# Performance work log

Hardware: AMD Instinct MI355X
Metric: run time of the kernel (lower is better)

## Reference

```python
import jax, jax.numpy as jnp
import numpy as np
from jax import lax

GAMMA = 1.0
BIG = 1e8  # matches the torch init value 100000000.0


def setup_inputs() -> dict:
    key = jax.random.key(0)
    k1, k2 = jax.random.split(key)
    B, n, m, d = 256, 256, 256, 32
    x = jax.random.normal(k1, (B, n, d), dtype=jnp.float32)
    y = jax.random.normal(k2, (B, m, d), dtype=jnp.float32)
    return {"x": x, "y": y}


def _soft_dtw(x, y, gamma):
    B, n, d = x.shape
    m = y.shape[1]
    # squared euclidean distances, (B, n, m); GEMM form avoids the (B,n,m,d) blowup
    x2 = jnp.sum(x * x, axis=-1)
    y2 = jnp.sum(y * y, axis=-1)
    dist = x2[:, :, None] + y2[:, None, :] - 2.0 * jnp.einsum('bnd,bmd->bnm', x, y)
    dist = jnp.maximum(dist, 0.0)  # cdist(p=2)**2 is nonnegative

    def softmin3(a, b, c):
        s = jnp.stack([a, b, c], axis=0)
        return -gamma * jax.nn.logsumexp(-s / gamma, axis=0)

    big_col = jnp.full((B,), BIG, dtype=x.dtype)

    def row_step(prev_row, d_row):
        # prev_row: (B, m+1) = D[i-1, :];  d_row: (B, m) = dist[:, i-1, :]
        def col_step(cur, inp):
            # cur: (B,) = D[i, j-1]; inp: (dist[i-1,j-1], D[i-1,j], D[i-1,j-1])
            dij, up, diag = inp
            new = dij + softmin3(up, cur, diag)
            return new, new
        xs = (d_row.T, prev_row[:, 1:].T, prev_row[:, :-1].T)  # each (m, B)
        _, vals = lax.scan(col_step, big_col, xs)  # vals: (m, B)
        new_row = jnp.concatenate([big_col[:, None], vals.T], axis=1)  # (B, m+1)
        return new_row, None

    init_row = jnp.concatenate(
        [jnp.zeros((B, 1), x.dtype), jnp.full((B, m), BIG, dtype=x.dtype)], axis=1)
    final_row, _ = lax.scan(row_step, init_row, jnp.swapaxes(dist, 0, 1))  # scan over n rows
    return jnp.mean(final_row[:, m])


def reference(x, y):
    return _soft_dtw(x, y, GAMMA)
```

## Files before the change

kernel.cpp:

```cpp
#include <hip/hip_runtime.h>

#define BIG 1e8f
#define LN2 0.69314718f
#define LOG2E 1.44269504f
#define M2L -2.8853900818f

#define RSLOT 112
#define DRB 1040

#define OFF_XH   116480
#define OFF_X2S  132864
#define OFF_Y2S  133888
#define OFF_RDY  134912
#define OFF_PRG  134976
#define LDS_BYTES 135040

typedef _Float16 half8 __attribute__((ext_vector_type(8)));
typedef _Float16 half2_t __attribute__((ext_vector_type(2)));
typedef float f32x4 __attribute__((ext_vector_type(4)));

__device__ __forceinline__ float exp2g(float x) {
#if __has_builtin(__builtin_amdgcn_exp2f)
    return __builtin_amdgcn_exp2f(x);
#else
    return exp2f(x);
#endif
}
__device__ __forceinline__ float log2g(float x) {
#if __has_builtin(__builtin_amdgcn_logf)
    return __builtin_amdgcn_logf(x);
#else
    return log2f(x);
#endif
}

__device__ __forceinline__ half2_t pkrtz(float a, float b) {
    return __builtin_bit_cast(half2_t, __builtin_amdgcn_cvt_pkrtz(a, b));
}

__device__ __forceinline__ void pairp(float a, float b, float& m, float& s) {
    m = fminf(a, b);
    s = exp2g(-fabsf(a - b)) + 1.f;
}
__device__ __forceinline__ float smp(float m, float s, float v) {
    float d = v - m;
    float t = exp2g(-fabsf(d));
    float r = (d > 0.f) ? (t + s) : fmaf(s, t, 1.f);
    return fminf(m, v) - log2g(r);
}

__device__ __forceinline__ float shfl_up1(float v, float oldv) {
    int r = __builtin_amdgcn_update_dpp(
        __builtin_bit_cast(int, oldv), __builtin_bit_cast(int, v),
        0x138 , 0xf, 0xf, false);
    return __builtin_bit_cast(float, r);
}

__device__ __forceinline__ void dec2(unsigned int w, float& a, float& b) {
    half2_t h = __builtin_bit_cast(half2_t, w);
    a = (float)h[0];
    b = (float)h[1];
}

__global__ __launch_bounds__(128, 1) void sdtw_kernel(
    const float* __restrict__ x, const float* __restrict__ y,
    float* __restrict__ out) {
    extern __shared__ __align__(16) char smem[];
    unsigned char* band = (unsigned char*)smem;
    _Float16* xh = (_Float16*)(smem + OFF_XH);
    float* x2sL = (float*)(smem + OFF_X2S);
    float* y2sL = (float*)(smem + OFF_Y2S);
    volatile int* rdy = (volatile int*)(smem + OFF_RDY);
    volatile int* prg = (volatile int*)(smem + OFF_PRG);

    const int tid = threadIdx.x;
    const int b = blockIdx.x;
    const float* xb = x + (size_t)b * 8192;
    const float* yb = y + (size_t)b * 8192;

#pragma unroll
    for (int rr = 0; rr < 2; rr++) {
        const int r = tid + rr * 128;
        const float4* px = (const float4*)(xb + r * 32);
        union { _Float16 h[32]; half8 v[4]; } uc;
        float s2 = 0.f;
#pragma unroll
        for (int q = 0; q < 8; q++) {
            float4 f = px[q];
            s2 += f.x * f.x + f.y * f.y + f.z * f.z + f.w * f.w;
            uc.h[4 * q + 0] = (_Float16)f.x;
            uc.h[4 * q + 1] = (_Float16)f.y;
            uc.h[4 * q + 2] = (_Float16)f.z;
            uc.h[4 * q + 3] = (_Float16)f.w;
        }
        half8* dst = (half8*)&xh[r * 32];
#pragma unroll
        for (int q = 0; q < 4; q++) dst[q] = uc.v[q];
        x2sL[r] = s2 * LOG2E;

        const float4* py = (const float4*)(yb + r * 32);
        float t2 = 0.f;
#pragma unroll
        for (int q = 0; q < 8; q++) {
            float4 f = py[q];
            t2 += f.x * f.x + f.y * f.y + f.z * f.z + f.w * f.w;
        }
        y2sL[r] = t2 * LOG2E;
    }
    if (tid < 16) rdy[tid] = 0;
    if (tid == 16) *prg = 0;
    __syncthreads();

    if (tid >= 64) {
        const int lane = tid - 64;
        const int qd = lane >> 4, xr = lane & 15;

        half8 yfrag[16];
        float yvL[16];
#pragma unroll
        for (int ci = 0; ci < 16; ci++) {
            const float* yp = yb + (ci * 16 + xr) * 32 + qd * 8;
            float4 f0 = *(const float4*)yp;
            float4 f1 = *(const float4*)(yp + 4);
            half8 v;
            v[0] = (_Float16)f0.x; v[1] = (_Float16)f0.y;
            v[2] = (_Float16)f0.z; v[3] = (_Float16)f0.w;
            v[4] = (_Float16)f1.x; v[5] = (_Float16)f1.y;
            v[6] = (_Float16)f1.z; v[7] = (_Float16)f1.w;
            yfrag[ci] = v;
            yvL[ci] = y2sL[ci * 16 + xr];
        }

        for (int sg = 0; sg < 16; sg++) {
            if (sg >= 6) {
                const int need = 8 * sg - 40;
                while (*prg < need) {}
            }
            const half8 xf = *(const half8*)&xh[(sg * 16 + xr) * 32 + qd * 8];
            const float4 xl = *(const float4*)&x2sL[sg * 16 + qd * 4];
            const int p0 = 8 * sg + 2 * qd;
#pragma unroll
            for (int ci = 0; ci < 16; ci++) {
                f32x4 acc = {0.f, 0.f, 0.f, 0.f};
                acc = __builtin_amdgcn_mfma_f32_16x16x32_f16(xf, yfrag[ci], acc, 0, 0, 0);
                const int c = ci * 16 + xr;
                const float yv = yvL[ci];
                const float d0 = fmaxf(fmaf(M2L, acc[0], xl.x + yv), 0.f);
                const float d1 = fmaxf(fmaf(M2L, acc[1], xl.y + yv), 0.f);
                const float d2 = fmaxf(fmaf(M2L, acc[2], xl.z + yv), 0.f);
                const float d3 = fmaxf(fmaf(M2L, acc[3], xl.w + yv), 0.f);
                const half2_t h01 = pkrtz(d0, d1);
                const half2_t h23 = pkrtz(d2, d3);
                const int dr0 = p0 + (c >> 2);
                int s0_ = dr0;     if (s0_ >= RSLOT) s0_ -= RSLOT;
                int s1_ = dr0 + 1; if (s1_ >= RSLOT) s1_ -= RSLOT;
                *(half2_t*)&band[s0_ * DRB + 4 * c] = h01;
                *(half2_t*)&band[s1_ * DRB + 4 * c] = h23;
            }
            __threadfence_block();
            if (lane == 0) rdy[sg] = 1;
        }
        return;
    }

    const int lane = tid;
    float u0 = BIG, u1 = BIG, u2 = BIG, u3 = BIG, pA3 = BIG, pB3 = BIG;
    float G0 = (lane == 0) ? 0.f : BIG;
    float m0, s0, m1, s1, m2, s2, m3, s3;
    pairp(u0, G0, m0, s0);
    pairp(u1, u0, m1, s1);
    pairp(u2, u1, m2, s2);
    pairp(u3, u2, m3, s3);

    while (rdy[0] == 0) {}
    uint4 wreg = *(const uint4*)&band[16 * lane];

    for (int s_ = 1; s_ <= 191; s_++) {
        const float L0 = shfl_up1(pA3, BIG);
        const float L1 = shfl_up1(pB3, BIG);

        float dA0, dB0, dA1, dB1, dA2, dB2, dA3, dB3;
        dec2(wreg.x, dA0, dB0);
        dec2(wreg.y, dA1, dB1);
        dec2(wreg.z, dA2, dB2);
        dec2(wreg.w, dA3, dB3);

        const float A0 = dA0 + smp(m0, s0, L0);
        const float A1 = dA1 + smp(m1, s1, A0);
        const float A2 = dA2 + smp(m2, s2, A1);
        const float A3 = dA3 + smp(m3, s3, A2);

        if ((s_ & 7) == 0) {
            int st = s_ >> 3;
            if (st > 15) st = 15;
            while (rdy[st] == 0) {}
            if (lane == 0) *prg = s_;
        }
        int dn = (s_ > 190) ? 190 : s_;
        if (dn >= RSLOT) dn -= RSLOT;
        const uint4 wnext = *(const uint4*)&band[dn * DRB + 16 * lane];

        float n0, t0, n1, t1, n2, t2, n3, t3;
        pairp(A0, L0, n0, t0);
        pairp(A1, A0, n1, t1);
        pairp(A2, A1, n2, t2);
        pairp(A3, A2, n3, t3);
        const float B0 = dB0 + smp(n0, t0, L1);
        const float B1 = dB1 + smp(n1, t1, B0);
        const float B2 = dB2 + smp(n2, t2, B1);
        const float B3 = dB3 + smp(n3, t3, B2);

        const bool act = (unsigned)(s_ - lane - 1) < 128u;
        u0 = act ? B0 : u0;
        u1 = act ? B1 : u1;
        u2 = act ? B2 : u2;
        u3 = act ? B3 : u3;
        pA3 = act ? A3 : pA3;
        pB3 = act ? B3 : pB3;
        G0 = L1;
        pairp(u0, G0, m0, s0);
        pairp(u1, u0, m1, s1);
        pairp(u2, u1, m2, s2);
        pairp(u3, u2, m3, s3);
        wreg = wnext;
    }

    if (lane == 63) atomicAdd(out, u3 * (LN2 / 256.f));
}

extern "C" void kernel_launch(void* const* d_in, const int* in_sizes, int n_in,
                              void* d_out, int out_size, void* d_ws, size_t ws_size,
                              hipStream_t stream) {
    const float* x = (const float*)d_in[0];
    const float* y = (const float*)d_in[1];
    float* out = (float*)d_out;
    const int B = in_sizes[0] / (256 * 32);

    (void)hipFuncSetAttribute((const void*)sdtw_kernel,
                              hipFuncAttributeMaxDynamicSharedMemorySize,
                              LDS_BYTES);
    (void)hipMemsetAsync(d_out, 0, sizeof(float), stream);
    sdtw_kernel<<<dim3(B), dim3(128), LDS_BYTES, stream>>>(x, y, out);
}
```

Before: 136.7 us.

## Split DP wavefront across four waves with mailbox handoff and 8-bit distances

The single DP wave, which handled four columns per lane, is replaced by four waves, each owning a 64-column panel with one column per lane. The waves form a pipeline and pass boundary A/B values through an LDS mailbox polled with sentinel values. Distances are now quantized to 8-bit codes instead of fp16, so each panel fits in a full-size band buffer and the ring-buffer progress throttling is gone. The aim is to shorten the serial per-step dependency chain by spreading columns over more waves. In exchange it adds inter-wave spin-wait latency, pipeline fill skew and extra quantization error in the distances.

```diff
diff --git a/kernel.cpp b/kernel.cpp
--- a/kernel.cpp
+++ b/kernel.cpp
@@ -5,18 +5,22 @@
 #define LOG2E 1.44269504f
 #define M2L -2.8853900818f
 
-#define RSLOT 112
-#define DRB 1040
-
-#define OFF_XH   116480
-#define OFF_X2S  132864
-#define OFF_Y2S  133888
-#define OFF_RDY  134912
-#define OFF_PRG  134976
-#define LDS_BYTES 135040
+#define QE8 1.2259615f
+#define DD8 0.81568627f
+
+#define NDROW 193
+#define DRB 128
+#define PANEL (NDROW * DRB)
+#define SENT64 0x7F8000007F800000ULL
+
+#define OFF_XH   (4 * PANEL)
+#define OFF_X2S  (OFF_XH + 16384)
+#define OFF_Y2S  (OFF_X2S + 1024)
+#define OFF_MBOX (OFF_Y2S + 1024)
+#define OFF_RDY  (OFF_MBOX + 4608)
+#define LDS_BYTES (OFF_RDY + 256)
 
 typedef _Float16 half8 __attribute__((ext_vector_type(8)));
-typedef _Float16 half2_t __attribute__((ext_vector_type(2)));
 typedef float f32x4 __attribute__((ext_vector_type(4)));
 
 __device__ __forceinline__ float exp2g(float x) {
@@ -33,11 +37,6 @@
     return log2f(x);
 #endif
 }
-
-__device__ __forceinline__ half2_t pkrtz(float a, float b) {
-    return __builtin_bit_cast(half2_t, __builtin_amdgcn_cvt_pkrtz(a, b));
-}
-
 __device__ __forceinline__ void pairp(float a, float b, float& m, float& s) {
     m = fminf(a, b);
     s = exp2g(-fabsf(a - b)) + 1.f;
@@ -48,21 +47,17 @@
     float r = (d > 0.f) ? (t + s) : fmaf(s, t, 1.f);
     return fminf(m, v) - log2g(r);
 }
-
 __device__ __forceinline__ float shfl_up1(float v, float oldv) {
     int r = __builtin_amdgcn_update_dpp(
         __builtin_bit_cast(int, oldv), __builtin_bit_cast(int, v),
         0x138 , 0xf, 0xf, false);
     return __builtin_bit_cast(float, r);
 }
-
-__device__ __forceinline__ void dec2(unsigned int w, float& a, float& b) {
-    half2_t h = __builtin_bit_cast(half2_t, w);
-    a = (float)h[0];
-    b = (float)h[1];
-}
-
-__global__ __launch_bounds__(128, 1) void sdtw_kernel(
+__device__ __forceinline__ unsigned long long mread(const volatile unsigned long long* p) {
+    return *p;
+}
+
+__global__ __launch_bounds__(320, 1) void sdtw_kernel(
     const float* __restrict__ x, const float* __restrict__ y,
     float* __restrict__ out) {
     extern __shared__ __align__(16) char smem[];
@@ -70,17 +65,17 @@
     _Float16* xh = (_Float16*)(smem + OFF_XH);
     float* x2sL = (float*)(smem + OFF_X2S);
     float* y2sL = (float*)(smem + OFF_Y2S);
-    volatile int* rdy = (volatile int*)(smem + OFF_RDY);
-    volatile int* prg = (volatile int*)(smem + OFF_PRG);
+    volatile unsigned long long* mbox =
+        (volatile unsigned long long*)(smem + OFF_MBOX);
+    volatile int* rdyv = (volatile int*)(smem + OFF_RDY);
 
     const int tid = threadIdx.x;
     const int b = blockIdx.x;
     const float* xb = x + (size_t)b * 8192;
     const float* yb = y + (size_t)b * 8192;
 
-#pragma unroll
-    for (int rr = 0; rr < 2; rr++) {
-        const int r = tid + rr * 128;
+    if (tid < 256) {
+        const int r = tid;
         const float4* px = (const float4*)(xb + r * 32);
         union { _Float16 h[32]; half8 v[4]; } uc;
         float s2 = 0.f;
@@ -107,12 +102,13 @@
         }
         y2sL[r] = t2 * LOG2E;
     }
-    if (tid < 16) rdy[tid] = 0;
-    if (tid == 16) *prg = 0;
+    for (int i = tid; i < 576; i += 320)
+        *(volatile unsigned long long*)&mbox[i] = SENT64;
+    if (tid < 64) rdyv[tid] = 0;
     __syncthreads();
 
-    if (tid >= 64) {
-        const int lane = tid - 64;
+    if (tid >= 256) {
+        const int lane = tid - 256;
         const int qd = lane >> 4, xr = lane & 15;
 
         half8 yfrag[16];
@@ -132,100 +128,112 @@
         }
 
         for (int sg = 0; sg < 16; sg++) {
-            if (sg >= 6) {
-                const int need = 8 * sg - 40;
-                while (*prg < need) {}
-            }
             const half8 xf = *(const half8*)&xh[(sg * 16 + xr) * 32 + qd * 8];
             const float4 xl = *(const float4*)&x2sL[sg * 16 + qd * 4];
-            const int p0 = 8 * sg + 2 * qd;
-#pragma unroll
-            for (int ci = 0; ci < 16; ci++) {
-                f32x4 acc = {0.f, 0.f, 0.f, 0.f};
-                acc = __builtin_amdgcn_mfma_f32_16x16x32_f16(xf, yfrag[ci], acc, 0, 0, 0);
-                const int c = ci * 16 + xr;
-                const float yv = yvL[ci];
-                const float d0 = fmaxf(fmaf(M2L, acc[0], xl.x + yv), 0.f);
-                const float d1 = fmaxf(fmaf(M2L, acc[1], xl.y + yv), 0.f);
-                const float d2 = fmaxf(fmaf(M2L, acc[2], xl.z + yv), 0.f);
-                const float d3 = fmaxf(fmaf(M2L, acc[3], xl.w + yv), 0.f);
-                const half2_t h01 = pkrtz(d0, d1);
-                const half2_t h23 = pkrtz(d2, d3);
-                const int dr0 = p0 + (c >> 2);
-                int s0_ = dr0;     if (s0_ >= RSLOT) s0_ -= RSLOT;
-                int s1_ = dr0 + 1; if (s1_ >= RSLOT) s1_ -= RSLOT;
-                *(half2_t*)&band[s0_ * DRB + 4 * c] = h01;
-                *(half2_t*)&band[s1_ * DRB + 4 * c] = h23;
+#pragma unroll
+            for (int p = 0; p < 4; p++) {
+#pragma unroll
+                for (int j = 0; j < 4; j++) {
+                    const int ci = 4 * p + j;
+                    f32x4 acc = {0.f, 0.f, 0.f, 0.f};
+                    acc = __builtin_amdgcn_mfma_f32_16x16x32_f16(xf, yfrag[ci], acc, 0, 0, 0);
+                    const float yv = yvL[ci];
+                    float dv0 = fminf(fmaxf(fmaf(M2L, acc[0], xl.x + yv), 0.f) * QE8, 254.9f);
+                    float dv1 = fminf(fmaxf(fmaf(M2L, acc[1], xl.y + yv), 0.f) * QE8, 254.9f);
+                    float dv2 = fminf(fmaxf(fmaf(M2L, acc[2], xl.z + yv), 0.f) * QE8, 254.9f);
+                    float dv3 = fminf(fmaxf(fmaf(M2L, acc[3], xl.w + yv), 0.f) * QE8, 254.9f);
+                    const unsigned int q0 = (unsigned int)(dv0 + 0.5f);
+                    const unsigned int q1 = (unsigned int)(dv1 + 0.5f);
+                    const unsigned int q2 = (unsigned int)(dv2 + 0.5f);
+                    const unsigned int q3 = (unsigned int)(dv3 + 0.5f);
+                    const int cl = j * 16 + xr;
+                    const int dl0 = 8 * sg + 2 * qd + cl;
+                    unsigned char* pb = band + p * PANEL;
+                    *(unsigned short*)&pb[dl0 * DRB + 2 * cl] =
+                        (unsigned short)(q0 | (q1 << 8));
+                    *(unsigned short*)&pb[(dl0 + 1) * DRB + 2 * cl] =
+                        (unsigned short)(q2 | (q3 << 8));
+                }
+                __threadfence_block();
+                if (lane == 0) rdyv[p * 16 + sg] = 1;
             }
-            __threadfence_block();
-            if (lane == 0) rdy[sg] = 1;
         }
         return;
     }
 
-    const int lane = tid;
-    float u0 = BIG, u1 = BIG, u2 = BIG, u3 = BIG, pA3 = BIG, pB3 = BIG;
-    float G0 = (lane == 0) ? 0.f : BIG;
-    float m0, s0, m1, s1, m2, s2, m3, s3;
-    pairp(u0, G0, m0, s0);
-    pairp(u1, u0, m1, s1);
-    pairp(u2, u1, m2, s2);
-    pairp(u3, u2, m3, s3);
-
-    while (rdy[0] == 0) {}
-    uint4 wreg = *(const uint4*)&band[16 * lane];
-
-    for (int s_ = 1; s_ <= 191; s_++) {
-        const float L0 = shfl_up1(pA3, BIG);
-        const float L1 = shfl_up1(pB3, BIG);
-
-        float dA0, dB0, dA1, dB1, dA2, dB2, dA3, dB3;
-        dec2(wreg.x, dA0, dB0);
-        dec2(wreg.y, dA1, dB1);
-        dec2(wreg.z, dA2, dB2);
-        dec2(wreg.w, dA3, dB3);
-
-        const float A0 = dA0 + smp(m0, s0, L0);
-        const float A1 = dA1 + smp(m1, s1, A0);
-        const float A2 = dA2 + smp(m2, s2, A1);
-        const float A3 = dA3 + smp(m3, s3, A2);
-
-        if ((s_ & 7) == 0) {
-            int st = s_ >> 3;
+    const int w = tid >> 6;
+    const int lane = tid & 63;
+    const unsigned char* pb = band + w * PANEL;
+
+    float u = BIG, pA = BIG, pB = BIG;
+    float G0 = (tid == 0) ? 0.f : BIG;
+    float m0, s0;
+    pairp(u, G0, m0, s0);
+
+    while (rdyv[w * 16] == 0) {}
+    __threadfence_block();
+    unsigned short curw = *(const unsigned short*)&pb[0 * DRB + 2 * lane];
+
+    float bA[8], bB[8];
+    for (int k = 0; k < 24; k++) {
+        const int it0 = 8 * k;
+
+        if (w > 0 && k < 16) {
+            const volatile unsigned long long* mb = &mbox[(w - 1) * 192];
+            while (mread(&mb[it0 + 70]) == SENT64) {}
+#pragma unroll
+            for (int j = 0; j < 8; j++) {
+                const unsigned long long v = mread(&mb[it0 + 63 + j]);
+                bA[j] = __uint_as_float((unsigned int)v);
+                bB[j] = __uint_as_float((unsigned int)(v >> 32));
+            }
+        } else {
+#pragma unroll
+            for (int j = 0; j < 8; j++) { bA[j] = BIG; bB[j] = BIG; }
+        }
+        {
+            int st = k + 1;
             if (st > 15) st = 15;
-            while (rdy[st] == 0) {}
-            if (lane == 0) *prg = s_;
-        }
-        int dn = (s_ > 190) ? 190 : s_;
-        if (dn >= RSLOT) dn -= RSLOT;
-        const uint4 wnext = *(const uint4*)&band[dn * DRB + 16 * lane];
-
-        float n0, t0, n1, t1, n2, t2, n3, t3;
-        pairp(A0, L0, n0, t0);
-        pairp(A1, A0, n1, t1);
-        pairp(A2, A1, n2, t2);
-        pairp(A3, A2, n3, t3);
-        const float B0 = dB0 + smp(n0, t0, L1);
-        const float B1 = dB1 + smp(n1, t1, B0);
-        const float B2 = dB2 + smp(n2, t2, B1);
-        const float B3 = dB3 + smp(n3, t3, B2);
-
-        const bool act = (unsigned)(s_ - lane - 1) < 128u;
-        u0 = act ? B0 : u0;
-        u1 = act ? B1 : u1;
-        u2 = act ? B2 : u2;
-        u3 = act ? B3 : u3;
-        pA3 = act ? A3 : pA3;
-        pB3 = act ? B3 : pB3;
-        G0 = L1;
-        pairp(u0, G0, m0, s0);
-        pairp(u1, u0, m1, s1);
-        pairp(u2, u1, m2, s2);
-        pairp(u3, u2, m3, s3);
-        wreg = wnext;
+            while (rdyv[w * 16 + st] == 0) {}
+        }
+        __threadfence_block();
+
+#pragma unroll
+        for (int j = 0; j < 8; j++) {
+            const int it = it0 + j;
+
+            const float L0 = shfl_up1(pA, bA[j]);
+            const float L1 = shfl_up1(pB, bB[j]);
+
+            const float dA = (float)(curw & 255u) * DD8;
+            const float dB = (float)(curw >> 8) * DD8;
+
+            const unsigned short nw =
+                *(const unsigned short*)&pb[(it + 1) * DRB + 2 * lane];
+
+            const float A = dA + smp(m0, s0, L0);
+            float mL, sL;
+            pairp(L1, L0, mL, sL);
+            const float B = dB + smp(mL, sL, A);
+
+            const bool act = (unsigned int)(it - lane) < 128u;
+            u = act ? B : u;
+            pA = act ? A : pA;
+            pB = act ? B : pB;
+
+            if (w < 3 && lane == 63 && act)
+                *(volatile unsigned long long*)&mbox[w * 192 + it] =
+                    ((unsigned long long)__float_as_uint(B) << 32) |
+                    __float_as_uint(A);
+
+            G0 = L1;
+            pairp(u, G0, m0, s0);
+            curw = nw;
+        }
     }
 
-    if (lane == 63) atomicAdd(out, u3 * (LN2 / 256.f));
+    if (w == 3 && lane == 63)
+        atomicAdd(out, u * (LN2 / 256.f));
 }
 
 extern "C" void kernel_launch(void* const* d_in, const int* in_sizes, int n_in,
@@ -240,5 +248,5 @@
                               hipFuncAttributeMaxDynamicSharedMemorySize,
                               LDS_BYTES);
     (void)hipMemsetAsync(d_out, 0, sizeof(float), stream);
-    sdtw_kernel<<<dim3(B), dim3(128), LDS_BYTES, stream>>>(x, y, out);
-}
+    sdtw_kernel<<<dim3(B), dim3(320), LDS_BYTES, stream>>>(x, y, out);
+}
```

Result: slower. 149.0 us (+9.0%).

## Represent soft-DTW cells as min-shift plus scaled probability to drop per-cell log

Applied to the files above, without the earlier changes.

Each DP cell is now stored as a pair: a shift S (hard-min path of dist plus min of neighbours) and a linear-domain weight P. The recurrence then propagates P with exp2 coefficients and FMAs instead of computing a log2 per cell, and a single log is taken only at the final cell. This removes the per-cell logarithm and the pairwise precomputation from the serial dependency chain. In exchange it doubles register state and shuffles, adds more exp2 calls, and risks P underflowing, since the hard-min shift can drift away from the true soft value over long paths.

```diff
diff --git a/kernel.cpp b/kernel.cpp
--- a/kernel.cpp
+++ b/kernel.cpp
@@ -1,6 +1,7 @@
 #include <hip/hip_runtime.h>
 
 #define BIG 1e8f
+#define DEADS 1e9f
 #define LN2 0.69314718f
 #define LOG2E 1.44269504f
 #define M2L -2.8853900818f
@@ -33,29 +34,18 @@
     return log2f(x);
 #endif
 }
-
 __device__ __forceinline__ half2_t pkrtz(float a, float b) {
     return __builtin_bit_cast(half2_t, __builtin_amdgcn_cvt_pkrtz(a, b));
 }
-
-__device__ __forceinline__ void pairp(float a, float b, float& m, float& s) {
-    m = fminf(a, b);
-    s = exp2g(-fabsf(a - b)) + 1.f;
-}
-__device__ __forceinline__ float smp(float m, float s, float v) {
-    float d = v - m;
-    float t = exp2g(-fabsf(d));
-    float r = (d > 0.f) ? (t + s) : fmaf(s, t, 1.f);
-    return fminf(m, v) - log2g(r);
-}
-
+__device__ __forceinline__ float coef(float arg) {
+    return exp2g(fminf(arg, 0.f));
+}
 __device__ __forceinline__ float shfl_up1(float v, float oldv) {
     int r = __builtin_amdgcn_update_dpp(
         __builtin_bit_cast(int, oldv), __builtin_bit_cast(int, v),
         0x138 , 0xf, 0xf, false);
     return __builtin_bit_cast(float, r);
 }
-
 __device__ __forceinline__ void dec2(unsigned int w, float& a, float& b) {
     half2_t h = __builtin_bit_cast(half2_t, w);
     a = (float)h[0];
@@ -164,20 +154,20 @@
     }
 
     const int lane = tid;
-    float u0 = BIG, u1 = BIG, u2 = BIG, u3 = BIG, pA3 = BIG, pB3 = BIG;
-    float G0 = (lane == 0) ? 0.f : BIG;
-    float m0, s0, m1, s1, m2, s2, m3, s3;
-    pairp(u0, G0, m0, s0);
-    pairp(u1, u0, m1, s1);
-    pairp(u2, u1, m2, s2);
-    pairp(u3, u2, m3, s3);
+    float uP0 = 0.f, uP1 = 0.f, uP2 = 0.f, uP3 = 0.f;
+    float uS0 = DEADS, uS1 = DEADS, uS2 = DEADS, uS3 = DEADS;
+    float pA3P = 0.f, pA3S = DEADS, pB3P = 0.f, pB3S = DEADS;
+    float GP = (lane == 0) ? 1.f : 0.f;
+    float GS = (lane == 0) ? 0.f : DEADS;
 
     while (rdy[0] == 0) {}
     uint4 wreg = *(const uint4*)&band[16 * lane];
 
     for (int s_ = 1; s_ <= 191; s_++) {
-        const float L0 = shfl_up1(pA3, BIG);
-        const float L1 = shfl_up1(pB3, BIG);
+        const float LP0 = shfl_up1(pA3P, 0.f);
+        const float LS0 = shfl_up1(pA3S, DEADS);
+        const float LP1 = shfl_up1(pB3P, 0.f);
+        const float LS1 = shfl_up1(pB3S, DEADS);
 
         float dA0, dB0, dA1, dB1, dA2, dB2, dA3, dB3;
         dec2(wreg.x, dA0, dB0);
@@ -185,11 +175,6 @@
         dec2(wreg.z, dA2, dB2);
         dec2(wreg.w, dA3, dB3);
 
-        const float A0 = dA0 + smp(m0, s0, L0);
-        const float A1 = dA1 + smp(m1, s1, A0);
-        const float A2 = dA2 + smp(m2, s2, A1);
-        const float A3 = dA3 + smp(m3, s3, A2);
-
         if ((s_ & 7) == 0) {
             int st = s_ >> 3;
             if (st > 15) st = 15;
@@ -200,32 +185,61 @@
         if (dn >= RSLOT) dn -= RSLOT;
         const uint4 wnext = *(const uint4*)&band[dn * DRB + 16 * lane];
 
-        float n0, t0, n1, t1, n2, t2, n3, t3;
-        pairp(A0, L0, n0, t0);
-        pairp(A1, A0, n1, t1);
-        pairp(A2, A1, n2, t2);
-        pairp(A3, A2, n3, t3);
-        const float B0 = dB0 + smp(n0, t0, L1);
-        const float B1 = dB1 + smp(n1, t1, B0);
-        const float B2 = dB2 + smp(n2, t2, B1);
-        const float B3 = dB3 + smp(n3, t3, B2);
+        const float A0 = dA0 + fminf(fminf(uS0, GS), LS0);
+        const float A1 = dA1 + fminf(fminf(uS1, uS0), A0);
+        const float A2 = dA2 + fminf(fminf(uS2, uS1), A1);
+        const float A3 = dA3 + fminf(fminf(uS3, uS2), A2);
+        const float k0 = A0 - dA0, k1 = A1 - dA1, k2 = A2 - dA2, k3 = A3 - dA3;
+
+        const float bA0 = coef(k0 - uS0) * uP0 + coef(k0 - GS) * GP;
+        const float bA1 = coef(k1 - uS1) * uP1 + coef(k1 - uS0) * uP0;
+        const float bA2 = coef(k2 - uS2) * uP2 + coef(k2 - uS1) * uP1;
+        const float bA3 = coef(k3 - uS3) * uP3 + coef(k3 - uS2) * uP2;
+        const float cl0 = coef(k0 - LS0);
+        const float cl1 = coef(k1 - A0);
+        const float cl2 = coef(k2 - A1);
+        const float cl3 = coef(k3 - A2);
+
+        const float PA0 = fmaf(cl0, LP0, bA0);
+        const float PA1 = fmaf(cl1, PA0, bA1);
+        const float PA2 = fmaf(cl2, PA1, bA2);
+        const float PA3 = fmaf(cl3, PA2, bA3);
+
+        const float SB0 = dB0 + fminf(fminf(A0, LS0), LS1);
+        const float SB1 = dB1 + fminf(fminf(A1, A0), SB0);
+        const float SB2 = dB2 + fminf(fminf(A2, A1), SB1);
+        const float SB3 = dB3 + fminf(fminf(A3, A2), SB2);
+        const float q0 = SB0 - dB0, q1 = SB1 - dB1, q2 = SB2 - dB2, q3 = SB3 - dB3;
+
+        const float bB0 = coef(q0 - A0) * PA0 + coef(q0 - LS0) * LP0;
+        const float bB1 = coef(q1 - A1) * PA1 + coef(q1 - A0) * PA0;
+        const float bB2 = coef(q2 - A2) * PA2 + coef(q2 - A1) * PA1;
+        const float bB3 = coef(q3 - A3) * PA3 + coef(q3 - A2) * PA2;
+        const float e0 = coef(q0 - LS1);
+        const float e1 = coef(q1 - SB0);
+        const float e2 = coef(q2 - SB1);
+        const float e3 = coef(q3 - SB2);
+
+        const float PB0 = fmaf(e0, LP1, bB0);
+        const float PB1 = fmaf(e1, PB0, bB1);
+        const float PB2 = fmaf(e2, PB1, bB2);
+        const float PB3 = fmaf(e3, PB2, bB3);
 
         const bool act = (unsigned)(s_ - lane - 1) < 128u;
-        u0 = act ? B0 : u0;
-        u1 = act ? B1 : u1;
-        u2 = act ? B2 : u2;
-        u3 = act ? B3 : u3;
-        pA3 = act ? A3 : pA3;
-        pB3 = act ? B3 : pB3;
-        G0 = L1;
-        pairp(u0, G0, m0, s0);
-        pairp(u1, u0, m1, s1);
-        pairp(u2, u1, m2, s2);
-        pairp(u3, u2, m3, s3);
+        uP0 = act ? PB0 : uP0;  uS0 = act ? SB0 : uS0;
+        uP1 = act ? PB1 : uP1;  uS1 = act ? SB1 : uS1;
+        uP2 = act ? PB2 : uP2;  uS2 = act ? SB2 : uS2;
+        uP3 = act ? PB3 : uP3;  uS3 = act ? SB3 : uS3;
+        pA3P = act ? PA3 : pA3P;  pA3S = act ? A3 : pA3S;
+        pB3P = act ? PB3 : pB3P;  pB3S = act ? SB3 : pB3S;
+        GP = LP1;  GS = LS1;
         wreg = wnext;
     }
 
-    if (lane == 63) atomicAdd(out, u3 * (LN2 / 256.f));
+    if (lane == 63) {
+        const float v = uS3 - log2g(uP3);
+        atomicAdd(out, v * (LN2 / 256.f));
+    }
 }
 
 extern "C" void kernel_launch(void* const* d_in, const int* in_sizes, int n_in,
```

Result: slower. 141.6 us (+3.5%).
